# Kernel optimization log

Hardware: AMD Instinct MI355X
Metric: run time of the kernel (lower is better)

Reference implementation:

```python
import jax, jax.numpy as jnp
import numpy as np

D = 64            # number of devices (leaves hold D/8 each)
B = 65536         # batch of states
FEAT = 5 + 4 * D  # 261
HID = 128


def setup_inputs() -> dict:
    key = jax.random.key(0)
    ks = jax.random.split(key, 10)
    def nrm(k, shape, s=0.1):
        return jax.random.normal(k, shape, jnp.float32) * s
    return {
        "x": jax.random.normal(ks[0], (B, FEAT), jnp.float32),
        # gate params per depth d: 2^d nodes, weight dim 5 + 4*D/2^d
        "w0": nrm(ks[1], (1, 5 + 4 * D)),
        "b0": jnp.zeros((1,), jnp.float32),
        "w1": nrm(ks[2], (2, 5 + 4 * (D // 2))),
        "b1": jnp.zeros((2,), jnp.float32),
        "w2": nrm(ks[3], (4, 5 + 4 * (D // 4))),
        "b2": jnp.zeros((4,), jnp.float32),
        # leaf prob_dist (torch inits to zeros; random here for a non-trivial baseline)
        "leaf_probs": nrm(ks[4], (8, D // 8), 1.0),
        # critic MLP
        "Wc1": nrm(ks[5], (FEAT, HID)),
        "bc1": jnp.zeros((HID,), jnp.float32),
        "Wc2": nrm(ks[6], (HID, 1)),
        "bc2": jnp.zeros((1,), jnp.float32),
    }


def reference(x, w0, b0, w1, b1, w2, b2, leaf_probs, Wc1, bc1, Wc2, bc2):
    # Batched deterministic ClusterTree routing (exploration disabled).
    x5 = x[:, :5]                       # (B, 5) global features
    dev = x[:, 5:].reshape(B, D, 4)     # (B, D, 4) per-device features
    node = jnp.zeros((B,), jnp.int32)   # current node index at each depth
    cum = jnp.ones((B,), x.dtype)       # product of gate values along path
    for d, (wd, bd) in enumerate([(w0, b0), (w1, b1), (w2, b2)]):
        nd = D >> d                     # devices per node at this depth
        off = node * nd                 # contiguous-cluster start offset
        idx = off[:, None] + jnp.arange(nd)                     # (B, nd)
        dslice = jnp.take_along_axis(dev, idx[:, :, None], 1)   # (B, nd, 4)
        w = wd[node]                    # (B, 5 + 4*nd)
        gate = (jnp.sum(x5 * w[:, :5], -1)
                + jnp.sum(dslice.reshape(B, -1) * w[:, 5:], -1)
                + bd[node])
        val = jax.nn.sigmoid(gate)
        cum = cum * val                 # torch: val * child_output, recursively
        node = node * 2 + (val >= 0.5).astype(jnp.int32)
    p = cum[:, None] * leaf_probs[node]                 # (B, D//8)
    v = jax.nn.relu(x @ Wc1 + bc1) @ Wc2 + bc2          # (B, 1) critic
    return p, v
```

## Files before the change

### kernel.cpp

```cpp
#include <hip/hip_runtime.h>
#include <hip/hip_bf16.h>
#include <stdint.h>

#define NB    65536
#define FEATN 261
#define HIDN  128
#define ROWS  64
#define NSTEP 17
#define SROW  296
#define NTHR  256

typedef __attribute__((ext_vector_type(8)))  short bf16x8;
typedef __attribute__((ext_vector_type(16))) float f32x16;

#define MFMA32(A, B, C) __builtin_amdgcn_mfma_f32_32x32x16_bf16(A, B, C, 0, 0, 0)

__global__ void prep_B(const float* __restrict__ Wc1, uint16_t* __restrict__ wsB) {
    int t = blockIdx.x * blockDim.x + threadIdx.x;
    if (t >= NSTEP * 4 * 64) return;
    int p = t >> 6, l = t & 63;
    int s = p >> 2, nt = p & 3;
    int n = nt * 32 + (l & 31);
    int kb = 16 * s + 8 * (l >> 5);
    uint16_t hw[8];
    #pragma unroll
    for (int j = 0; j < 8; ++j) {
        int k = kb + j;
        float v = (k < FEATN) ? Wc1[(size_t)k * HIDN + n] : 0.f;
        __hip_bfloat16 b = __float2bfloat16(v);
        hw[j] = *reinterpret_cast<uint16_t*>(&b);
    }
    *reinterpret_cast<uint4*>(wsB + (size_t)p * 512 + l * 8) =
        *reinterpret_cast<uint4*>(hw);
}

__global__ __launch_bounds__(NTHR, 3) void ac_fused(
    const float* __restrict__ x,
    const float* __restrict__ w0, const float* __restrict__ b0,
    const float* __restrict__ w1, const float* __restrict__ b1,
    const float* __restrict__ w2, const float* __restrict__ b2,
    const float* __restrict__ leaf,
    const uint16_t* __restrict__ wsB,
    const float* __restrict__ bc1, const float* __restrict__ Wc2,
    const float* __restrict__ bc2,
    float* __restrict__ out_p, float* __restrict__ out_v)
{
    __shared__ uint16_t Axs[ROWS * SROW];
    __shared__ float bc1s[HIDN];
    __shared__ float wc2s[HIDN];
    __shared__ float vpart[ROWS * 2];

    const int tid = threadIdx.x;
    const int rowBase = blockIdx.x * ROWS;

    if (tid < HIDN) { bc1s[tid] = bc1[tid]; wc2s[tid] = Wc2[tid]; }
    if (tid < ROWS) {
        uint16_t* rp = Axs + tid * SROW;
        rp[261] = 0;
        *reinterpret_cast<uint32_t*>(rp + 262) = 0u;
        uint4 z; z.x = z.y = z.z = z.w = 0u;
        *reinterpret_cast<uint4*>(rp + 264) = z;
        *reinterpret_cast<uint4*>(rp + 272) = z;
        *reinterpret_cast<uint4*>(rp + 280) = z;
        *reinterpret_cast<uint4*>(rp + 288) = z;
    }

    {
        const float4* xg4 = reinterpret_cast<const float4*>(x + (size_t)rowBase * FEATN);
        for (int i = tid; i < ROWS * FEATN / 4; i += NTHR) {
            float4 v = xg4[i];
            const float* vv = reinterpret_cast<const float*>(&v);
            int f = i << 2;
            int m = f / FEATN;
            int k = f - m * FEATN;
            if (k + 3 < FEATN) {
                uint16_t* dst = Axs + m * SROW + k;
                #pragma unroll
                for (int j = 0; j < 4; ++j) {
                    __hip_bfloat16 b = __float2bfloat16(vv[j]);
                    dst[j] = *reinterpret_cast<uint16_t*>(&b);
                }
            } else {
                #pragma unroll
                for (int j = 0; j < 4; ++j) {
                    if (k >= FEATN) { k -= FEATN; m++; }
                    __hip_bfloat16 b = __float2bfloat16(vv[j]);
                    Axs[m * SROW + k] = *reinterpret_cast<uint16_t*>(&b);
                    k++;
                }
            }
        }
    }

    {
        const int s = tid & 15;

        float w0s[17];
        #pragma unroll
        for (int j = 0; j < 16; ++j) w0s[j] = w0[s + 16 * j];
        w0s[16] = (s < 5) ? w0[256 + s] : 0.f;

        float w1a[9], w1b[9];
        #pragma unroll
        for (int j = 0; j < 8; ++j) {
            w1a[j] = w1[s + 16 * j];
            w1b[j] = w1[133 + s + 16 * j];
        }
        w1a[8] = (s < 5) ? w1[128 + s]       : 0.f;
        w1b[8] = (s < 5) ? w1[133 + 128 + s] : 0.f;

        #pragma unroll
        for (int pass = 0; pass < 4; ++pass) {
            const int rloc = pass * 16 + (tid >> 4);
            const float* xr = x + (size_t)(rowBase + rloc) * FEATN;

            float xv[17];
            #pragma unroll
            for (int j = 0; j < 16; ++j) xv[j] = xr[s + 16 * j];
            xv[16] = (s < 5) ? xr[256 + s] : 0.f;
            float part = 0.f;
            #pragma unroll
            for (int j = 0; j < 17; ++j) part += xv[j] * w0s[j];
            part += __shfl_xor(part, 1);
            part += __shfl_xor(part, 2);
            part += __shfl_xor(part, 4);
            part += __shfl_xor(part, 8);
            float gate = part + b0[0];
            int node = (gate >= 0.f) ? 1 : 0;
            float cum = 1.f / (1.f + __expf(-gate));

            {
                const float* p = xr + node * 128 + s;
                float xw[9];
                xw[0] = (s < 5) ? xr[s] : p[0];
                #pragma unroll
                for (int j = 1; j < 8; ++j) xw[j] = p[16 * j];
                xw[8] = (s < 5) ? p[128] : 0.f;
                part = 0.f;
                #pragma unroll
                for (int j = 0; j < 9; ++j)
                    part += xw[j] * (node ? w1b[j] : w1a[j]);
                part += __shfl_xor(part, 1);
                part += __shfl_xor(part, 2);
                part += __shfl_xor(part, 4);
                part += __shfl_xor(part, 8);
                gate = part + b1[node];
                cum *= 1.f / (1.f + __expf(-gate));
                node = node * 2 + ((gate >= 0.f) ? 1 : 0);
            }
            {
                const float* w2r = w2 + node * 69;
                const float* p2  = xr + node * 64 + s;
                float xw[5], ww[5];
                xw[0] = (s < 5) ? xr[s] : p2[0];
                ww[0] = w2r[s];
                #pragma unroll
                for (int j = 1; j < 4; ++j) { xw[j] = p2[16 * j]; ww[j] = w2r[s + 16 * j]; }
                xw[4] = (s < 5) ? p2[64]      : 0.f;
                ww[4] = (s < 5) ? w2r[64 + s] : 0.f;
                part = 0.f;
                #pragma unroll
                for (int j = 0; j < 5; ++j) part += xw[j] * ww[j];
                part += __shfl_xor(part, 1);
                part += __shfl_xor(part, 2);
                part += __shfl_xor(part, 4);
                part += __shfl_xor(part, 8);
                gate = part + b2[node];
                cum *= 1.f / (1.f + __expf(-gate));
                node = node * 2 + ((gate >= 0.f) ? 1 : 0);
            }
            if (s < 8)
                out_p[(size_t)(rowBase + rloc) * 8 + s] = cum * leaf[node * 8 + s];
        }
    }

    __syncthreads();

    const int lane = tid & 63;
    const int w    = tid >> 6;
    const int mt   = w >> 1;
    const int nh   = w & 1;

    f32x16 acc0 = {}, acc1 = {};
    const uint16_t* arow = Axs + (mt * 32 + (lane & 31)) * SROW + (lane >> 5) * 8;
    const uint16_t* bgl  = wsB + (size_t)(2 * nh) * 512 + lane * 8;

    bf16x8 ca[4], cb0[4], cb1[4];
    bf16x8 na[4], nb0[4], nb1[4];
    #pragma unroll
    for (int d = 0; d < 4; ++d) {
        ca[d]  = *reinterpret_cast<const bf16x8*>(arow + d * 16);
        cb0[d] = *reinterpret_cast<const bf16x8*>(bgl + (size_t)(d * 4)     * 512);
        cb1[d] = *reinterpret_cast<const bf16x8*>(bgl + (size_t)(d * 4 + 1) * 512);
    }
    #pragma unroll
    for (int g = 0; g < 4; ++g) {
        if (g < 3) {
            #pragma unroll
            for (int d = 0; d < 4; ++d) {
                const int st = (g + 1) * 4 + d;
                na[d]  = *reinterpret_cast<const bf16x8*>(arow + st * 16);
                nb0[d] = *reinterpret_cast<const bf16x8*>(bgl + (size_t)(st * 4)     * 512);
                nb1[d] = *reinterpret_cast<const bf16x8*>(bgl + (size_t)(st * 4 + 1) * 512);
            }
        } else {
            na[0]  = *reinterpret_cast<const bf16x8*>(arow + 16 * 16);
            nb0[0] = *reinterpret_cast<const bf16x8*>(bgl + (size_t)(16 * 4)     * 512);
            nb1[0] = *reinterpret_cast<const bf16x8*>(bgl + (size_t)(16 * 4 + 1) * 512);
        }
        #pragma unroll
        for (int d = 0; d < 4; ++d) {
            acc0 = MFMA32(ca[d], cb0[d], acc0);
            acc1 = MFMA32(ca[d], cb1[d], acc1);
        }
        #pragma unroll
        for (int d = 0; d < 4; ++d) { ca[d] = na[d]; cb0[d] = nb0[d]; cb1[d] = nb1[d]; }
    }
    acc0 = MFMA32(ca[0], cb0[0], acc0);
    acc1 = MFMA32(ca[0], cb1[0], acc1);

    {
        const int c = lane & 31;
        const int q = lane >> 5;
        const int n0 = 2 * nh * 32 + c;
        const int n1 = n0 + 32;
        const float bb0 = bc1s[n0], ww0 = wc2s[n0];
        const float bb1 = bc1s[n1], ww1 = wc2s[n1];

        float pv[16];
        #pragma unroll
        for (int reg = 0; reg < 16; ++reg) {
            float h0 = acc0[reg] + bb0; h0 = h0 > 0.f ? h0 : 0.f;
            float h1 = acc1[reg] + bb1; h1 = h1 > 0.f ? h1 : 0.f;
            float t = h0 * ww0 + h1 * ww1;
            t += __shfl_xor(t, 1);
            t += __shfl_xor(t, 2);
            t += __shfl_xor(t, 4);
            t += __shfl_xor(t, 8);
            t += __shfl_xor(t, 16);
            pv[reg] = t;
        }
        #pragma unroll
        for (int reg = 0; reg < 16; ++reg) {
            if (c == reg) {
                int row_local = (reg & 3) + 8 * (reg >> 2) + 4 * q;
                vpart[(mt * 32 + row_local) * 2 + nh] = pv[reg];
            }
        }
    }
    __syncthreads();
    if (tid < ROWS)
        out_v[rowBase + tid] = vpart[tid * 2] + vpart[tid * 2 + 1] + bc2[0];
}

extern "C" void kernel_launch(void* const* d_in, const int* in_sizes, int n_in,
                              void* d_out, int out_size, void* d_ws, size_t ws_size,
                              hipStream_t stream) {
    const float* x    = (const float*)d_in[0];
    const float* w0   = (const float*)d_in[1];
    const float* b0   = (const float*)d_in[2];
    const float* w1   = (const float*)d_in[3];
    const float* b1   = (const float*)d_in[4];
    const float* w2   = (const float*)d_in[5];
    const float* b2   = (const float*)d_in[6];
    const float* leaf = (const float*)d_in[7];
    const float* Wc1  = (const float*)d_in[8];
    const float* bc1  = (const float*)d_in[9];
    const float* Wc2  = (const float*)d_in[10];
    const float* bc2  = (const float*)d_in[11];

    uint16_t* wsB = (uint16_t*)d_ws;

    float* out_p = (float*)d_out;
    float* out_v = out_p + (size_t)NB * 8;

    prep_B<<<(NSTEP * 4 * 64 + 255) / 256, 256, 0, stream>>>(Wc1, wsB);
    ac_fused<<<NB / ROWS, NTHR, 0, stream>>>(
        x, w0, b0, w1, b1, w2, b2, leaf, wsB, bc1, Wc2, bc2, out_p, out_v);
}
```

Before: 141.0 us.

## Split tree routing and critic GEMM into separate kernels with vectorized gate loads

Moves the tree-gate routing out of the fused kernel into its own lightweight kernel. There, each 16-lane group handles one row using float4 loads of x and the gate weights, with the per-node weight choice done by register selects. The critic GEMM becomes a separate kernel that processes 128 rows per 512-thread block, with a shallower 2-step prefetch pipeline in its MFMA loop. The aim is to stop the serial, latency-bound routing passes from stalling the MFMA work and to raise occupancy for both parts. The cost is an extra launch and reading x from memory twice.

```diff
diff --git a/kernel.cpp b/kernel.cpp
--- a/kernel.cpp
+++ b/kernel.cpp
@@ -5,13 +5,15 @@
 #define NB    65536
 #define FEATN 261
 #define HIDN  128
-#define ROWS  64
 #define NSTEP 17
 #define SROW  296
-#define NTHR  256
+
+#define ROWSG 128
+#define NTHRG 512
 
 typedef __attribute__((ext_vector_type(8)))  short bf16x8;
 typedef __attribute__((ext_vector_type(16))) float f32x16;
+typedef float f32x4u __attribute__((ext_vector_type(4), aligned(4)));
 
 #define MFMA32(A, B, C) __builtin_amdgcn_mfma_f32_32x32x16_bf16(A, B, C, 0, 0, 0)
 
@@ -34,27 +36,122 @@
         *reinterpret_cast<uint4*>(hw);
 }
 
-__global__ __launch_bounds__(NTHR, 3) void ac_fused(
+__global__ void tree_kernel(
     const float* __restrict__ x,
     const float* __restrict__ w0, const float* __restrict__ b0,
     const float* __restrict__ w1, const float* __restrict__ b1,
     const float* __restrict__ w2, const float* __restrict__ b2,
     const float* __restrict__ leaf,
+    float* __restrict__ out_p)
+{
+    const int tid = threadIdx.x;
+    const int s   = tid & 15;
+    const int row = blockIdx.x * 16 + (tid >> 4);
+    const float* xr = x + (size_t)row * FEATN;
+
+    f32x4u w0q[4];
+    #pragma unroll
+    for (int j = 0; j < 4; ++j)
+        w0q[j] = *reinterpret_cast<const f32x4u*>(w0 + 4 * s + 64 * j);
+    const float w0t = (s < 5) ? w0[256 + s] : 0.f;
+
+    f32x4u w1aq[2], w1bq[2];
+    #pragma unroll
+    for (int j = 0; j < 2; ++j) {
+        w1aq[j] = *reinterpret_cast<const f32x4u*>(w1 + 5 + 8 * s + 4 * j);
+        w1bq[j] = *reinterpret_cast<const f32x4u*>(w1 + 133 + 5 + 8 * s + 4 * j);
+    }
+    const float w1a5 = (s < 5) ? w1[s]       : 0.f;
+    const float w1b5 = (s < 5) ? w1[133 + s] : 0.f;
+
+    f32x4u w2q0 = *reinterpret_cast<const f32x4u*>(w2 +  0 * 69 + 5 + 4 * s);
+    f32x4u w2q1 = *reinterpret_cast<const f32x4u*>(w2 +  1 * 69 + 5 + 4 * s);
+    f32x4u w2q2 = *reinterpret_cast<const f32x4u*>(w2 +  2 * 69 + 5 + 4 * s);
+    f32x4u w2q3 = *reinterpret_cast<const f32x4u*>(w2 +  3 * 69 + 5 + 4 * s);
+    float w25_0 = (s < 5) ? w2[0 * 69 + s] : 0.f;
+    float w25_1 = (s < 5) ? w2[1 * 69 + s] : 0.f;
+    float w25_2 = (s < 5) ? w2[2 * 69 + s] : 0.f;
+    float w25_3 = (s < 5) ? w2[3 * 69 + s] : 0.f;
+
+    f32x4u xq[4];
+    #pragma unroll
+    for (int j = 0; j < 4; ++j)
+        xq[j] = *reinterpret_cast<const f32x4u*>(xr + 4 * s + 64 * j);
+    const float xt  = (s < 5) ? xr[256 + s] : 0.f;
+    const float xs5 = (s < 5) ? xr[s]       : 0.f;
+
+    float part = xt * w0t;
+    #pragma unroll
+    for (int j = 0; j < 4; ++j)
+        #pragma unroll
+        for (int c = 0; c < 4; ++c)
+            part += xq[j][c] * w0q[j][c];
+    part += __shfl_xor(part, 1);
+    part += __shfl_xor(part, 2);
+    part += __shfl_xor(part, 4);
+    part += __shfl_xor(part, 8);
+    float gate = part + b0[0];
+    int node = (gate >= 0.f) ? 1 : 0;
+    float cum = 1.f / (1.f + __expf(-gate));
+
+    {
+        const float* base = xr + 5 + 128 * node + 8 * s;
+        f32x4u xw0 = *reinterpret_cast<const f32x4u*>(base);
+        f32x4u xw1 = *reinterpret_cast<const f32x4u*>(base + 4);
+        part = xs5 * (node ? w1b5 : w1a5);
+        #pragma unroll
+        for (int c = 0; c < 4; ++c) {
+            part += xw0[c] * (node ? w1bq[0][c] : w1aq[0][c]);
+            part += xw1[c] * (node ? w1bq[1][c] : w1aq[1][c]);
+        }
+        part += __shfl_xor(part, 1);
+        part += __shfl_xor(part, 2);
+        part += __shfl_xor(part, 4);
+        part += __shfl_xor(part, 8);
+        gate = part + b1[node];
+        cum *= 1.f / (1.f + __expf(-gate));
+        node = node * 2 + ((gate >= 0.f) ? 1 : 0);
+    }
+    {
+        f32x4u xv2 = *reinterpret_cast<const f32x4u*>(xr + 5 + 64 * node + 4 * s);
+        f32x4u t0 = (node & 1) ? w2q1 : w2q0;
+        f32x4u t1 = (node & 1) ? w2q3 : w2q2;
+        f32x4u wsel = (node & 2) ? t1 : t0;
+        float w5a = (node & 1) ? w25_1 : w25_0;
+        float w5b = (node & 1) ? w25_3 : w25_2;
+        float w5sel = (node & 2) ? w5b : w5a;
+        part = xs5 * w5sel;
+        #pragma unroll
+        for (int c = 0; c < 4; ++c) part += xv2[c] * wsel[c];
+        part += __shfl_xor(part, 1);
+        part += __shfl_xor(part, 2);
+        part += __shfl_xor(part, 4);
+        part += __shfl_xor(part, 8);
+        gate = part + b2[node];
+        cum *= 1.f / (1.f + __expf(-gate));
+        node = node * 2 + ((gate >= 0.f) ? 1 : 0);
+    }
+    if (s < 8)
+        out_p[(size_t)row * 8 + s] = cum * leaf[node * 8 + s];
+}
+
+__global__ __launch_bounds__(NTHRG, 4) void critic_gemm(
+    const float* __restrict__ x,
     const uint16_t* __restrict__ wsB,
     const float* __restrict__ bc1, const float* __restrict__ Wc2,
     const float* __restrict__ bc2,
-    float* __restrict__ out_p, float* __restrict__ out_v)
+    float* __restrict__ out_v)
 {
-    __shared__ uint16_t Axs[ROWS * SROW];
+    __shared__ uint16_t Axs[ROWSG * SROW];
     __shared__ float bc1s[HIDN];
     __shared__ float wc2s[HIDN];
-    __shared__ float vpart[ROWS * 2];
+    __shared__ float vpart[ROWSG * 2];
 
     const int tid = threadIdx.x;
-    const int rowBase = blockIdx.x * ROWS;
+    const int rowBase = blockIdx.x * ROWSG;
 
     if (tid < HIDN) { bc1s[tid] = bc1[tid]; wc2s[tid] = Wc2[tid]; }
-    if (tid < ROWS) {
+    if (tid < ROWSG) {
         uint16_t* rp = Axs + tid * SROW;
         rp[261] = 0;
         *reinterpret_cast<uint32_t*>(rp + 262) = 0u;
@@ -67,7 +164,7 @@
 
     {
         const float4* xg4 = reinterpret_cast<const float4*>(x + (size_t)rowBase * FEATN);
-        for (int i = tid; i < ROWS * FEATN / 4; i += NTHR) {
+        for (int i = tid; i < ROWSG * FEATN / 4; i += NTHRG) {
             float4 v = xg4[i];
             const float* vv = reinterpret_cast<const float*>(&v);
             int f = i << 2;
@@ -91,89 +188,6 @@
             }
         }
     }
-
-    {
-        const int s = tid & 15;
-
-        float w0s[17];
-        #pragma unroll
-        for (int j = 0; j < 16; ++j) w0s[j] = w0[s + 16 * j];
-        w0s[16] = (s < 5) ? w0[256 + s] : 0.f;
-
-        float w1a[9], w1b[9];
-        #pragma unroll
-        for (int j = 0; j < 8; ++j) {
-            w1a[j] = w1[s + 16 * j];
-            w1b[j] = w1[133 + s + 16 * j];
-        }
-        w1a[8] = (s < 5) ? w1[128 + s]       : 0.f;
-        w1b[8] = (s < 5) ? w1[133 + 128 + s] : 0.f;
-
-        #pragma unroll
-        for (int pass = 0; pass < 4; ++pass) {
-            const int rloc = pass * 16 + (tid >> 4);
-            const float* xr = x + (size_t)(rowBase + rloc) * FEATN;
-
-            float xv[17];
-            #pragma unroll
-            for (int j = 0; j < 16; ++j) xv[j] = xr[s + 16 * j];
-            xv[16] = (s < 5) ? xr[256 + s] : 0.f;
-            float part = 0.f;
-            #pragma unroll
-            for (int j = 0; j < 17; ++j) part += xv[j] * w0s[j];
-            part += __shfl_xor(part, 1);
-            part += __shfl_xor(part, 2);
-            part += __shfl_xor(part, 4);
-            part += __shfl_xor(part, 8);
-            float gate = part + b0[0];
-            int node = (gate >= 0.f) ? 1 : 0;
-            float cum = 1.f / (1.f + __expf(-gate));
-
-            {
-                const float* p = xr + node * 128 + s;
-                float xw[9];
-                xw[0] = (s < 5) ? xr[s] : p[0];
-                #pragma unroll
-                for (int j = 1; j < 8; ++j) xw[j] = p[16 * j];
-                xw[8] = (s < 5) ? p[128] : 0.f;
-                part = 0.f;
-                #pragma unroll
-                for (int j = 0; j < 9; ++j)
-                    part += xw[j] * (node ? w1b[j] : w1a[j]);
-                part += __shfl_xor(part, 1);
-                part += __shfl_xor(part, 2);
-                part += __shfl_xor(part, 4);
-                part += __shfl_xor(part, 8);
-                gate = part + b1[node];
-                cum *= 1.f / (1.f + __expf(-gate));
-                node = node * 2 + ((gate >= 0.f) ? 1 : 0);
-            }
-            {
-                const float* w2r = w2 + node * 69;
-                const float* p2  = xr + node * 64 + s;
-                float xw[5], ww[5];
-                xw[0] = (s < 5) ? xr[s] : p2[0];
-                ww[0] = w2r[s];
-                #pragma unroll
-                for (int j = 1; j < 4; ++j) { xw[j] = p2[16 * j]; ww[j] = w2r[s + 16 * j]; }
-                xw[4] = (s < 5) ? p2[64]      : 0.f;
-                ww[4] = (s < 5) ? w2r[64 + s] : 0.f;
-                part = 0.f;
-                #pragma unroll
-                for (int j = 0; j < 5; ++j) part += xw[j] * ww[j];
-                part += __shfl_xor(part, 1);
-                part += __shfl_xor(part, 2);
-                part += __shfl_xor(part, 4);
-                part += __shfl_xor(part, 8);
-                gate = part + b2[node];
-                cum *= 1.f / (1.f + __expf(-gate));
-                node = node * 2 + ((gate >= 0.f) ? 1 : 0);
-            }
-            if (s < 8)
-                out_p[(size_t)(rowBase + rloc) * 8 + s] = cum * leaf[node * 8 + s];
-        }
-    }
-
     __syncthreads();
 
     const int lane = tid & 63;
@@ -185,20 +199,19 @@
     const uint16_t* arow = Axs + (mt * 32 + (lane & 31)) * SROW + (lane >> 5) * 8;
     const uint16_t* bgl  = wsB + (size_t)(2 * nh) * 512 + lane * 8;
 
-    bf16x8 ca[4], cb0[4], cb1[4];
-    bf16x8 na[4], nb0[4], nb1[4];
-    #pragma unroll
-    for (int d = 0; d < 4; ++d) {
+    bf16x8 ca[2], cb0[2], cb1[2], na[2], nb0[2], nb1[2];
+    #pragma unroll
+    for (int d = 0; d < 2; ++d) {
         ca[d]  = *reinterpret_cast<const bf16x8*>(arow + d * 16);
         cb0[d] = *reinterpret_cast<const bf16x8*>(bgl + (size_t)(d * 4)     * 512);
         cb1[d] = *reinterpret_cast<const bf16x8*>(bgl + (size_t)(d * 4 + 1) * 512);
     }
     #pragma unroll
-    for (int g = 0; g < 4; ++g) {
-        if (g < 3) {
+    for (int g = 0; g < 8; ++g) {
+        if (g < 7) {
             #pragma unroll
-            for (int d = 0; d < 4; ++d) {
-                const int st = (g + 1) * 4 + d;
+            for (int d = 0; d < 2; ++d) {
+                const int st = 2 * g + 2 + d;
                 na[d]  = *reinterpret_cast<const bf16x8*>(arow + st * 16);
                 nb0[d] = *reinterpret_cast<const bf16x8*>(bgl + (size_t)(st * 4)     * 512);
                 nb1[d] = *reinterpret_cast<const bf16x8*>(bgl + (size_t)(st * 4 + 1) * 512);
@@ -209,12 +222,12 @@
             nb1[0] = *reinterpret_cast<const bf16x8*>(bgl + (size_t)(16 * 4 + 1) * 512);
         }
         #pragma unroll
-        for (int d = 0; d < 4; ++d) {
+        for (int d = 0; d < 2; ++d) {
             acc0 = MFMA32(ca[d], cb0[d], acc0);
             acc1 = MFMA32(ca[d], cb1[d], acc1);
         }
         #pragma unroll
-        for (int d = 0; d < 4; ++d) { ca[d] = na[d]; cb0[d] = nb0[d]; cb1[d] = nb1[d]; }
+        for (int d = 0; d < 2; ++d) { ca[d] = na[d]; cb0[d] = nb0[d]; cb1[d] = nb1[d]; }
     }
     acc0 = MFMA32(ca[0], cb0[0], acc0);
     acc1 = MFMA32(ca[0], cb1[0], acc1);
@@ -249,7 +262,7 @@
         }
     }
     __syncthreads();
-    if (tid < ROWS)
+    if (tid < ROWSG)
         out_v[rowBase + tid] = vpart[tid * 2] + vpart[tid * 2 + 1] + bc2[0];
 }
 
@@ -275,6 +288,8 @@
     float* out_v = out_p + (size_t)NB * 8;
 
     prep_B<<<(NSTEP * 4 * 64 + 255) / 256, 256, 0, stream>>>(Wc1, wsB);
-    ac_fused<<<NB / ROWS, NTHR, 0, stream>>>(
-        x, w0, b0, w1, b1, w2, b2, leaf, wsB, bc1, Wc2, bc2, out_p, out_v);
-}
+    tree_kernel<<<NB / 16, 256, 0, stream>>>(
+        x, w0, b0, w1, b1, w2, b2, leaf, out_p);
+    critic_gemm<<<NB / ROWSG, NTHRG, 0, stream>>>(
+        x, wsB, bc1, Wc2, bc2, out_v);
+}
```

After: 141.5 us. About the same (+0.4%).
